# Performance work log

Hardware: AMD Instinct MI355X
Metric: run time of the kernel (lower is better)

## Reference

```python
import jax, jax.numpy as jnp
import numpy as np

H = 256      # hidden_size
B = 32       # batch
T = 4096     # timesteps / graph nodes
E = 8192     # edges per graph
PATH = 1
EXPAND_WEIGHT = 0.1
MODE = 'son'


def setup_inputs() -> dict:
    key = jax.random.key(0)
    ks = jax.random.split(key, 6)
    hidden = jax.random.normal(ks[0], (B, H), jnp.float32)
    encoder_outputs = jax.random.normal(ks[1], (T, B, H), jnp.float32)
    edges_src = jax.random.randint(ks[2], (B, E), 0, T)
    edges_dst = jax.random.randint(ks[3], (B, E), 0, T)
    # nn.Linear(2H, 2H) params (kaiming-uniform-ish scale) and the v vector
    lim = 1.0 / np.sqrt(2 * H)
    W_attn = jax.random.uniform(ks[4], (2 * H, 2 * H), jnp.float32, -lim, lim)
    b_attn = jnp.zeros((2 * H,), jnp.float32)
    v = jax.random.uniform(ks[5], (2 * H,), jnp.float32, -lim, lim)
    return {"hidden": hidden, "encoder_outputs": encoder_outputs,
            "edges_src": edges_src, "edges_dst": edges_dst,
            "W_attn": W_attn, "b_attn": b_attn, "v": v}


def reference(hidden, encoder_outputs, edges_src, edges_dst, W_attn, b_attn, v):
    Bb, Hh = hidden.shape
    Tt = encoder_outputs.shape[0]
    # h: [B, T, H] (hidden repeated over timesteps); enc: [B, T, H]
    h = jnp.broadcast_to(hidden[:, None, :], (Bb, Tt, Hh))
    enc = jnp.transpose(encoder_outputs, (1, 0, 2))
    # score: tanh(Linear(cat)) then v . energy -> [B, T]
    energy = jnp.tanh(jnp.concatenate([h, enc], axis=2) @ W_attn.T + b_attn)
    scores = jnp.einsum('btd,d->bt', energy, v)
    w = jax.nn.softmax(scores, axis=1)
    # expand_attn: scatter-add along graph edges, skipping consecutive (y == x+1)
    mask = (edges_dst != edges_src + 1).astype(w.dtype)  # [B, E]
    def scatter(wb, src, dst, m):
        if MODE == 'son':
            return jnp.zeros_like(wb).at[dst].add(wb[src] * m)
        else:
            return jnp.zeros_like(wb).at[src].add(wb[dst] * m)
    for _ in range(PATH):
        w = jax.vmap(scatter)(w, edges_src, edges_dst, mask) * EXPAND_WEIGHT
    return w[:, None, :]  # [B, 1, T]
```

## Files before the change

### kernel.cpp

```cpp
#include <hip/hip_runtime.h>
#include <hip/hip_bf16.h>

typedef __attribute__((ext_vector_type(8))) short bf16x8;
typedef __attribute__((ext_vector_type(4))) float f32x4;

#define HD 256
#define NB 32
#define NT 4096
#define NE 8192
#define N2 512

static __device__ __forceinline__ unsigned short f2bf(float f) {
  unsigned int u = __float_as_uint(f);
  u += 0x7fff + ((u >> 16) & 1);
  return (unsigned short)(u >> 16);
}
static __device__ __forceinline__ short4 cvt4(float4 a) {
  return make_short4((short)f2bf(a.x), (short)f2bf(a.y),
                     (short)f2bf(a.z), (short)f2bf(a.w));
}
static __device__ __forceinline__ float fast_tanh(float x) {
  float e = __builtin_amdgcn_exp2f(x * 2.8853900817779268f);
  return __builtin_fmaf(-2.f, __builtin_amdgcn_rcpf(e + 1.f), 1.f);
}
static __device__ __forceinline__ bf16x8 pack8(float4 a, float4 b) {
  union { bf16x8 v; unsigned int u[4]; } r;
  r.u[0] = (__float_as_uint(a.y) & 0xffff0000u) | (__float_as_uint(a.x) >> 16);
  r.u[1] = (__float_as_uint(a.w) & 0xffff0000u) | (__float_as_uint(a.z) >> 16);
  r.u[2] = (__float_as_uint(b.y) & 0xffff0000u) | (__float_as_uint(b.x) >> 16);
  r.u[3] = (__float_as_uint(b.w) & 0xffff0000u) | (__float_as_uint(b.z) >> 16);
  return r.v;
}

#define GLDS16(g, l)                                                       \
  __builtin_amdgcn_global_load_lds(                                        \
      (const __attribute__((address_space(1))) unsigned int*)(g),          \
      (__attribute__((address_space(3))) unsigned int*)(l), 16, 0, 0)

__global__ __launch_bounds__(256) void prep(
    const float* __restrict__ hidden, const float* __restrict__ Wattn,
    const float* __restrict__ battn, float* __restrict__ cvecT,
    short* __restrict__ Wbf) {
  const int tid = threadIdx.x;
  if (blockIdx.x < 256) {
    __shared__ float Ws[64 * 260];
    __shared__ float Hs[HD];
    const int chunk = blockIdx.x & 7;
    const int b = blockIdx.x >> 3;
#pragma unroll
    for (int it = 0; it < 16; ++it) {
      int f = it * 1024 + tid * 4;
      int i = f >> 8, k = f & 255;
      float4 w4 = *(const float4*)(Wattn + (chunk * 64 + i) * N2 + k);
      *(float4*)&Ws[i * 260 + k] = w4;
    }
    if (tid < 64)
      *(float4*)&Hs[tid * 4] = *(const float4*)(hidden + b * HD + tid * 4);
    __syncthreads();
    const int nl = tid >> 2;
    const int kb = (tid & 3) * 64;
    float sum = 0.f;
#pragma unroll
    for (int z = 0; z < 64; z += 4) {
      float4 h4 = *(const float4*)&Hs[kb + z];
      float4 w4 = *(const float4*)&Ws[nl * 260 + kb + z];
      sum = fmaf(h4.x, w4.x, sum);
      sum = fmaf(h4.y, w4.y, sum);
      sum = fmaf(h4.z, w4.z, sum);
      sum = fmaf(h4.w, w4.w, sum);
    }
    sum += __shfl_xor(sum, 1, 64);
    sum += __shfl_xor(sum, 2, 64);
    if ((tid & 3) == 0)
      cvecT[(chunk * 64 + nl) * NB + b] = sum + battn[chunk * 64 + nl];
  } else {
    int f = (blockIdx.x - 256) * 1024 + tid * 4;
    int n = f >> 8, k = f & 255;
    float4 w4 = *(const float4*)(Wattn + n * N2 + HD + k);
    *(short4*)(Wbf + f) = cvt4(w4);
  }
}

static __device__ __forceinline__ void bload(bf16x8* dst, const short* __restrict__ Wbf,
                                             int nbase, int q, int kk) {
#pragma unroll
  for (int nf = 0; nf < 8; ++nf)
    dst[nf] = *(const bf16x8*)(Wbf + (nbase + nf * 16) * HD + kk * 32 + q * 8);
}

static __device__ __forceinline__ void kstep(f32x4 acc[4][8], const float4* As4,
                                             const bf16x8* b, int m, int q, int ks) {
#pragma unroll
  for (int mi = 0; mi < 4; ++mi) {
    const int r = mi * 16 + m;
    const int cb = r * 64 + ks * 8;
    float4 a0 = As4[cb + ((2 * q) ^ (r & 7))];
    float4 a1 = As4[cb + ((2 * q + 1) ^ (r & 7))];
    bf16x8 af = pack8(a0, a1);
#pragma unroll
    for (int nf = 0; nf < 8; ++nf)
      acc[mi][nf] =
          __builtin_amdgcn_mfma_f32_16x16x32_bf16(af, b[nf], acc[mi][nf], 0, 0, 0);
  }
}

__global__ __launch_bounds__(256, 2) void score_gemm(
    const float* __restrict__ enc, const short* __restrict__ Wbf,
    const float* __restrict__ cvecT, const float* __restrict__ vvec,
    float* __restrict__ scores) {
  __shared__ float4 As4[64 * 64];
  __shared__ float part[4][64];
  const int tid = threadIdx.x;
  const int w = tid >> 6, lane = tid & 63, q = lane >> 4, m = lane & 15;
  const int row0 = blockIdx.x * 64;

#pragma unroll
  for (int i = 0; i < 16; ++i) {
    const int r = i * 4 + w;
    const int gc = (lane & ~7) | ((lane & 7) ^ (r & 7));
    GLDS16(enc + (row0 + r) * HD + gc * 4, &As4[r * 64]);
  }

  f32x4 acc[4][8];
#pragma unroll
  for (int mi = 0; mi < 4; ++mi)
#pragma unroll
    for (int nf = 0; nf < 8; ++nf) acc[mi][nf] = (f32x4){0.f, 0.f, 0.f, 0.f};

  const int nbase = w * 128 + m;
  bf16x8 b0[8], b1[8];
  bload(b0, Wbf, nbase, q, 0);

  __syncthreads();

#pragma unroll 1
  for (int ks2 = 0; ks2 < 4; ++ks2) {
    const int ks = ks2 * 2;
    bload(b1, Wbf, nbase, q, ks + 1);
    kstep(acc, As4, b0, m, q, ks);
    if (ks2 < 3) bload(b0, Wbf, nbase, q, ks + 2);
    kstep(acc, As4, b1, m, q, ks + 1);
  }

  float p[4][4];
#pragma unroll
  for (int mi = 0; mi < 4; ++mi)
#pragma unroll
    for (int j = 0; j < 4; ++j) p[mi][j] = 0.f;

#pragma unroll
  for (int nf = 0; nf < 8; ++nf) {
    const int n = w * 128 + nf * 16 + m;
    const float vv = vvec[n];
    const f32x4 cvA = *(const f32x4*)(cvecT + n * NB + 4 * q);
    const f32x4 cvB = *(const f32x4*)(cvecT + n * NB + 16 + 4 * q);
#pragma unroll
    for (int mi = 0; mi < 4; ++mi) {
      const f32x4 cv = (mi & 1) ? cvB : cvA;
#pragma unroll
      for (int j = 0; j < 4; ++j)
        p[mi][j] += fast_tanh(acc[mi][nf][j] + cv[j]) * vv;
    }
  }
#pragma unroll
  for (int mi = 0; mi < 4; ++mi) {
#pragma unroll
    for (int j = 0; j < 4; ++j) {
      float e = p[mi][j];
      e += __shfl_xor(e, 1, 64);
      e += __shfl_xor(e, 2, 64);
      e += __shfl_xor(e, 4, 64);
      e += __shfl_xor(e, 8, 64);
      if (m == 0) part[w][mi * 16 + 4 * q + j] = e;
    }
  }
  __syncthreads();
  if (tid < 64) {
    const int r = row0 + tid;
    scores[(r & 31) * NT + (r >> 5)] =
        part[0][tid] + part[1][tid] + part[2][tid] + part[3][tid];
  }
}

__global__ __launch_bounds__(1024) void softmax_scatter(
    const float* __restrict__ sc, const int* __restrict__ esrc,
    const int* __restrict__ edst, float* __restrict__ out) {
  __shared__ float wls[NT];
  __shared__ float accs[NT];
  __shared__ float rtmp[16];
  __shared__ float rmax, rinv;
  const int b = blockIdx.x;
  const int tid = threadIdx.x;
  const int wid = tid >> 6, lane = tid & 63;

  float s[4];
  float mx = -1e30f;
#pragma unroll
  for (int p = 0; p < 4; ++p) {
    s[p] = sc[b * NT + tid + p * 1024];
    mx = fmaxf(mx, s[p]);
  }
#pragma unroll
  for (int d = 32; d >= 1; d >>= 1) mx = fmaxf(mx, __shfl_xor(mx, d, 64));
  if (lane == 0) rtmp[wid] = mx;
  __syncthreads();
  if (tid == 0) {
    float mm = rtmp[0];
#pragma unroll
    for (int i = 1; i < 16; ++i) mm = fmaxf(mm, rtmp[i]);
    rmax = mm;
  }
  __syncthreads();
  mx = rmax;
  float e[4];
  float sm = 0.f;
#pragma unroll
  for (int p = 0; p < 4; ++p) {
    e[p] = __expf(s[p] - mx);
    sm += e[p];
  }
#pragma unroll
  for (int d = 32; d >= 1; d >>= 1) sm += __shfl_xor(sm, d, 64);
  if (lane == 0) rtmp[wid] = sm;
  __syncthreads();
  if (tid == 0) {
    float tt = 0.f;
#pragma unroll
    for (int i = 0; i < 16; ++i) tt += rtmp[i];
    rinv = 0.1f / tt;
  }
  __syncthreads();
  const float inv = rinv;
#pragma unroll
  for (int p = 0; p < 4; ++p) {
    wls[tid + p * 1024] = e[p] * inv;
    accs[tid + p * 1024] = 0.f;
  }
  __syncthreads();
#pragma unroll
  for (int i = 0; i < 8; ++i) {
    const int eid = b * NE + tid + i * 1024;
    const int ss = esrc[eid];
    const int dd = edst[eid];
    const float wv = wls[ss];
    if (dd != ss + 1) atomicAdd(&accs[dd], wv);
  }
  __syncthreads();
#pragma unroll
  for (int p = 0; p < 4; ++p)
    out[b * NT + tid + p * 1024] = accs[tid + p * 1024];
}

extern "C" void kernel_launch(void* const* d_in, const int* in_sizes, int n_in,
                              void* d_out, int out_size, void* d_ws, size_t ws_size,
                              hipStream_t stream) {
  const float* hidden = (const float*)d_in[0];
  const float* enc    = (const float*)d_in[1];
  const int*   esrc   = (const int*)d_in[2];
  const int*   edst   = (const int*)d_in[3];
  const float* Wattn  = (const float*)d_in[4];
  const float* battn  = (const float*)d_in[5];
  const float* vvec   = (const float*)d_in[6];
  float* out = (float*)d_out;

  char* ws = (char*)d_ws;
  float* cvecT  = (float*)ws;
  short* Wbf    = (short*)(ws + 65536);
  float* scores = (float*)(ws + 65536 + 262144);

  prep<<<384, 256, 0, stream>>>(hidden, Wattn, battn, cvecT, Wbf);
  score_gemm<<<(NB * NT) / 64, 256, 0, stream>>>(enc, Wbf, cvecT, vvec, scores);
  softmax_scatter<<<NB, 1024, 0, stream>>>(scores, esrc, edst, out);
}
```

Before: 284.4 us.

## Stage encoder tile as bf16 in LDS and split N across eight waves

The score GEMM now loads the fp32 encoder tile through registers, converts it to bf16 once, and stores it swizzled in LDS instead of using direct global-to-LDS fp32 copies. Each MFMA then reads its A fragment with a single 16-byte LDS load rather than two loads plus a repack in every k-step. Blocks grow to 512 threads with eight waves, each covering 64 output columns, which halves per-wave accumulators and B registers and is meant to raise occupancy. The tradeoff is that the global load goes through registers instead of async LDS copies, and the final reduction now spans eight partial sums.

```diff
diff --git a/kernel.cpp b/kernel.cpp
--- a/kernel.cpp
+++ b/kernel.cpp
@@ -31,11 +31,6 @@
   r.u[3] = (__float_as_uint(b.w) & 0xffff0000u) | (__float_as_uint(b.z) >> 16);
   return r.v;
 }
-
-#define GLDS16(g, l)                                                       \
-  __builtin_amdgcn_global_load_lds(                                        \
-      (const __attribute__((address_space(1))) unsigned int*)(g),          \
-      (__attribute__((address_space(3))) unsigned int*)(l), 16, 0, 0)
 
 __global__ __launch_bounds__(256) void prep(
     const float* __restrict__ hidden, const float* __restrict__ Wattn,
@@ -84,51 +79,54 @@
 static __device__ __forceinline__ void bload(bf16x8* dst, const short* __restrict__ Wbf,
                                              int nbase, int q, int kk) {
 #pragma unroll
-  for (int nf = 0; nf < 8; ++nf)
+  for (int nf = 0; nf < 4; ++nf)
     dst[nf] = *(const bf16x8*)(Wbf + (nbase + nf * 16) * HD + kk * 32 + q * 8);
 }
 
-static __device__ __forceinline__ void kstep(f32x4 acc[4][8], const float4* As4,
+static __device__ __forceinline__ void kstep(f32x4 acc[4][4], const short* Abf,
                                              const bf16x8* b, int m, int q, int ks) {
 #pragma unroll
   for (int mi = 0; mi < 4; ++mi) {
     const int r = mi * 16 + m;
-    const int cb = r * 64 + ks * 8;
-    float4 a0 = As4[cb + ((2 * q) ^ (r & 7))];
-    float4 a1 = As4[cb + ((2 * q + 1) ^ (r & 7))];
-    bf16x8 af = pack8(a0, a1);
-#pragma unroll
-    for (int nf = 0; nf < 8; ++nf)
+    const int cc = ks * 4 + q;
+    const int slot = (cc & ~7) | ((cc & 7) ^ (r & 7));
+    bf16x8 af = *(const bf16x8*)&Abf[r * 256 + slot * 8];
+#pragma unroll
+    for (int nf = 0; nf < 4; ++nf)
       acc[mi][nf] =
           __builtin_amdgcn_mfma_f32_16x16x32_bf16(af, b[nf], acc[mi][nf], 0, 0, 0);
   }
 }
 
-__global__ __launch_bounds__(256, 2) void score_gemm(
+__global__ __launch_bounds__(512, 4) void score_gemm(
     const float* __restrict__ enc, const short* __restrict__ Wbf,
     const float* __restrict__ cvecT, const float* __restrict__ vvec,
     float* __restrict__ scores) {
-  __shared__ float4 As4[64 * 64];
-  __shared__ float part[4][64];
+  __shared__ short Abf[64 * 256];
+  __shared__ float part[8][64];
   const int tid = threadIdx.x;
   const int w = tid >> 6, lane = tid & 63, q = lane >> 4, m = lane & 15;
   const int row0 = blockIdx.x * 64;
 
 #pragma unroll
-  for (int i = 0; i < 16; ++i) {
-    const int r = i * 4 + w;
-    const int gc = (lane & ~7) | ((lane & 7) ^ (r & 7));
-    GLDS16(enc + (row0 + r) * HD + gc * 4, &As4[r * 64]);
-  }
-
-  f32x4 acc[4][8];
+  for (int i = 0; i < 4; ++i) {
+    const int g = i * 512 + tid;
+    const int r = g >> 5, c = g & 31;
+    const float* src = enc + (row0 + r) * HD + c * 8;
+    float4 a0 = *(const float4*)src;
+    float4 a1 = *(const float4*)(src + 4);
+    const int slot = (c & ~7) | ((c & 7) ^ (r & 7));
+    *(bf16x8*)&Abf[r * 256 + slot * 8] = pack8(a0, a1);
+  }
+
+  f32x4 acc[4][4];
 #pragma unroll
   for (int mi = 0; mi < 4; ++mi)
 #pragma unroll
-    for (int nf = 0; nf < 8; ++nf) acc[mi][nf] = (f32x4){0.f, 0.f, 0.f, 0.f};
-
-  const int nbase = w * 128 + m;
-  bf16x8 b0[8], b1[8];
+    for (int nf = 0; nf < 4; ++nf) acc[mi][nf] = (f32x4){0.f, 0.f, 0.f, 0.f};
+
+  const int nbase = w * 64 + m;
+  bf16x8 b0[4], b1[4];
   bload(b0, Wbf, nbase, q, 0);
 
   __syncthreads();
@@ -137,9 +135,9 @@
   for (int ks2 = 0; ks2 < 4; ++ks2) {
     const int ks = ks2 * 2;
     bload(b1, Wbf, nbase, q, ks + 1);
-    kstep(acc, As4, b0, m, q, ks);
+    kstep(acc, Abf, b0, m, q, ks);
     if (ks2 < 3) bload(b0, Wbf, nbase, q, ks + 2);
-    kstep(acc, As4, b1, m, q, ks + 1);
+    kstep(acc, Abf, b1, m, q, ks + 1);
   }
 
   float p[4][4];
@@ -149,8 +147,8 @@
     for (int j = 0; j < 4; ++j) p[mi][j] = 0.f;
 
 #pragma unroll
-  for (int nf = 0; nf < 8; ++nf) {
-    const int n = w * 128 + nf * 16 + m;
+  for (int nf = 0; nf < 4; ++nf) {
+    const int n = w * 64 + nf * 16 + m;
     const float vv = vvec[n];
     const f32x4 cvA = *(const f32x4*)(cvecT + n * NB + 4 * q);
     const f32x4 cvB = *(const f32x4*)(cvecT + n * NB + 16 + 4 * q);
@@ -177,8 +175,10 @@
   __syncthreads();
   if (tid < 64) {
     const int r = row0 + tid;
-    scores[(r & 31) * NT + (r >> 5)] =
-        part[0][tid] + part[1][tid] + part[2][tid] + part[3][tid];
+    float s = 0.f;
+#pragma unroll
+    for (int ww = 0; ww < 8; ++ww) s += part[ww][tid];
+    scores[(r & 31) * NT + (r >> 5)] = s;
   }
 }
 
@@ -269,6 +269,6 @@
   float* scores = (float*)(ws + 65536 + 262144);
 
   prep<<<384, 256, 0, stream>>>(hidden, Wattn, battn, cvecT, Wbf);
-  score_gemm<<<(NB * NT) / 64, 256, 0, stream>>>(enc, Wbf, cvecT, vvec, scores);
+  score_gemm<<<(NB * NT) / 64, 512, 0, stream>>>(enc, Wbf, cvecT, vvec, scores);
   softmax_scatter<<<NB, 1024, 0, stream>>>(scores, esrc, edst, out);
 }
```

Measured after the change: 279.2 us. Within noise of the previous version (-1.8%).
